# Kernel optimization log

Measured on AMD Instinct MI355X. Metric: run time of the kernel, lower is better.

The kernel has to match this reference:

```python
import jax, jax.numpy as jnp
import numpy as np

N_NODES = 100000
N_EDGES = 3200000
NODE_DIM = 128
MRI_DIM, COG_DIM, CLIN_DIM, GEN_DIM = 256, 64, 32, 512
N_GRAPHS = 256
N_CLASSES = 3
HID = 16


def setup_inputs() -> dict:
    key = jax.random.key(0)
    ks = jax.random.split(key, 20)
    inp = {
        "x": jax.random.normal(ks[0], (N_NODES, NODE_DIM), jnp.float32),
        "edge_index": jax.random.randint(ks[1], (2, N_EDGES), 0, N_NODES, jnp.int64),
        "batch": jnp.sort(jax.random.randint(ks[2], (N_NODES,), 0, N_GRAPHS, jnp.int64)),
        "mri": jax.random.normal(ks[3], (N_GRAPHS, MRI_DIM), jnp.float32),
        "cog": jax.random.normal(ks[4], (N_GRAPHS, COG_DIM), jnp.float32),
        "clin": jax.random.normal(ks[5], (N_GRAPHS, CLIN_DIM), jnp.float32),
        "genetic": jax.random.normal(ks[6], (N_GRAPHS, GEN_DIM), jnp.float32),
        # GCNConv weight/bias
        "gcn_W": jax.random.normal(ks[7], (NODE_DIM, HID), jnp.float32) / np.sqrt(NODE_DIM),
        "gcn_b": jnp.zeros((HID,), jnp.float32),
        # modality FCs (each -> 4)
        "mri_W": jax.random.normal(ks[8], (MRI_DIM, 4), jnp.float32) / np.sqrt(MRI_DIM),
        "mri_b": jnp.zeros((4,), jnp.float32),
        "cog_W": jax.random.normal(ks[9], (COG_DIM, 4), jnp.float32) / np.sqrt(COG_DIM),
        "cog_b": jnp.zeros((4,), jnp.float32),
        "clin_W": jax.random.normal(ks[10], (CLIN_DIM, 4), jnp.float32) / np.sqrt(CLIN_DIM),
        "clin_b": jnp.zeros((4,), jnp.float32),
        "gen_W": jax.random.normal(ks[11], (GEN_DIM, 4), jnp.float32) / np.sqrt(GEN_DIM),
        "gen_b": jnp.zeros((4,), jnp.float32),
        # classifier: Linear(32,16) -> ReLU -> Dropout(eval: identity) -> Linear(16,3)
        "cls_W1": jax.random.normal(ks[12], (32, HID), jnp.float32) / np.sqrt(32.0),
        "cls_b1": jnp.zeros((HID,), jnp.float32),
        "cls_W2": jax.random.normal(ks[13], (HID, N_CLASSES), jnp.float32) / np.sqrt(HID),
        "cls_b2": jnp.zeros((N_CLASSES,), jnp.float32),
    }
    return inp


def gcn_conv(x, edge_index, W, b):
    # PyG GCNConv: add self-loops, symmetric normalization, scatter-add.
    n = x.shape[0]
    xw = x @ W  # [N, HID]
    loop = jnp.arange(n, dtype=edge_index.dtype)
    src = jnp.concatenate([edge_index[0], loop])
    dst = jnp.concatenate([edge_index[1], loop])
    deg = jax.ops.segment_sum(jnp.ones_like(dst, dtype=xw.dtype), dst, num_segments=n)
    dinv = jnp.where(deg > 0, jax.lax.rsqrt(deg), 0.0)
    norm = dinv[src] * dinv[dst]  # [E+N]
    msg = xw[src] * norm[:, None]  # gather + scale
    out = jax.ops.segment_sum(msg, dst, num_segments=n)  # scatter-add
    return out + b


def global_mean_pool(feat, batch, num_graphs):
    s = jax.ops.segment_sum(feat, batch, num_segments=num_graphs)
    cnt = jax.ops.segment_sum(jnp.ones((feat.shape[0],), feat.dtype), batch, num_segments=num_graphs)
    return s / jnp.maximum(cnt, 1.0)[:, None]


def reference(x, edge_index, batch, mri, cog, clin, genetic,
              gcn_W, gcn_b, mri_W, mri_b, cog_W, cog_b, clin_W, clin_b,
              gen_W, gen_b, cls_W1, cls_b1, cls_W2, cls_b2):
    g = jax.nn.relu(gcn_conv(x, edge_index, gcn_W, gcn_b))  # [N, 16]
    g_emb = global_mean_pool(g, batch, N_GRAPHS)            # [B, 16]
    m = jax.nn.relu(mri @ mri_W + mri_b)
    c = jax.nn.relu(cog @ cog_W + cog_b)
    cl = jax.nn.relu(clin @ clin_W + clin_b)
    ge = jax.nn.relu(genetic @ gen_W + gen_b)
    mm = jnp.concatenate([m, c, cl, ge], axis=1)            # [B, 16]
    comb = jnp.concatenate([g_emb, mm], axis=1)             # [B, 32]
    h = jax.nn.relu(comb @ cls_W1 + cls_b1)                 # dropout is identity in eval
    logits = h @ cls_W2 + cls_b2
    return jax.nn.log_softmax(logits, axis=1)
```

## Files before the change

kernel.cpp:

```cpp
#include <hip/hip_runtime.h>
#include <hip/hip_bf16.h>
#include <math.h>

#define N_NODES   100000
#define N_EDGES   3200000
#define NODE_DIM  128
#define HID       16
#define N_GRAPHS  256

#define BSHIFT    6
#define NPB       64
#define NBUCK     ((N_NODES + NPB - 1) >> BSHIFT)
#define NBLK      256
#define TOT       (NBUCK * NBLK)
#define ACC64S    9

#define FIX16  4096.0f
#define IFIX16 (1.0f/4096.0f)
#define FIXP   131072.0f
#define IFIXP  (1.0f/131072.0f)

__device__ __forceinline__ short f2bf(float f) {
    unsigned u = __float_as_uint(f);
    unsigned r = (u + 0x7FFF + ((u >> 16) & 1)) >> 16;
    return (short)r;
}
__device__ __forceinline__ int fx(float v, float s) { return __float2int_rn(v * s); }

__device__ __forceinline__ unsigned long long packA(int w) {
    return ((unsigned long long)(unsigned)(w >> 16) << 32)
         | (unsigned)((w & 0xFFFF) ^ 0x8000);
}

typedef __attribute__((ext_vector_type(8))) short bf16x8;
typedef __attribute__((ext_vector_type(4))) float f32x4;
typedef __attribute__((ext_vector_type(4))) int   i32x4;

__global__ __launch_bounds__(1024) void bucket_count(
    const int* __restrict__ dst, int* __restrict__ offT, int E, int chunk)
{
    __shared__ int cnt[NBUCK];
    const int t = threadIdx.x;
    const int b = (blockIdx.x & 7) * (NBLK >> 3) + (blockIdx.x >> 3);
    for (int k = t; k < NBUCK; k += 1024) cnt[k] = 0;
    __syncthreads();
    int e0 = b * chunk, e1 = min(E, e0 + chunk);
    if (e1 > e0) {
        const int4* d4 = (const int4*)dst;
        for (int i = (e0 >> 2) + t; i < (e1 >> 2); i += 1024) {
            int4 d = d4[i];
            atomicAdd(&cnt[d.x >> BSHIFT], 1);
            atomicAdd(&cnt[d.y >> BSHIFT], 1);
            atomicAdd(&cnt[d.z >> BSHIFT], 1);
            atomicAdd(&cnt[d.w >> BSHIFT], 1);
        }
    }
    __syncthreads();
    for (int k = t; k < NBUCK; k += 1024) offT[k * NBLK + b] = cnt[k];
}

__global__ __launch_bounds__(256) void scan_blocksum(
    const int* __restrict__ M, int* __restrict__ bsum, int n)
{
    __shared__ int red[256];
    int t = threadIdx.x;
    int base = blockIdx.x * 2048 + t * 8;
    int s = 0;
    #pragma unroll
    for (int k = 0; k < 8; ++k) { int i = base + k; if (i < n) s += M[i]; }
    red[t] = s; __syncthreads();
    for (int o = 128; o > 0; o >>= 1) {
        if (t < o) red[t] += red[t + o];
        __syncthreads();
    }
    if (t == 0) bsum[blockIdx.x] = red[0];
}

__global__ __launch_bounds__(256) void scan_write2(
    int* __restrict__ M, const int* __restrict__ bsum, int n, int nb)
{
    __shared__ int tmp[256];
    __shared__ int tsum[256];
    int t = threadIdx.x;
    tmp[t] = (t < nb) ? bsum[t] : 0;
    __syncthreads();
    for (int o = 1; o < 256; o <<= 1) {
        int a = (t >= o) ? tmp[t - o] : 0;
        __syncthreads();
        tmp[t] += a;
        __syncthreads();
    }
    const int pre0 = (blockIdx.x > 0) ? tmp[blockIdx.x - 1] : 0;

    int base = blockIdx.x * 2048 + t * 8;
    int v[8]; int s = 0;
    #pragma unroll
    for (int k = 0; k < 8; ++k) { int i = base + k; v[k] = (i < n) ? M[i] : 0; s += v[k]; }
    tsum[t] = s; __syncthreads();
    int mine = s;
    for (int o = 1; o < 256; o <<= 1) {
        int a = (t >= o) ? tsum[t - o] : 0;
        __syncthreads();
        tsum[t] += a;
        __syncthreads();
    }
    int pre = pre0 + tsum[t] - mine;
    #pragma unroll
    for (int k = 0; k < 8; ++k) {
        int i = base + k;
        if (i < n) { M[i] = pre; pre += v[k]; }
    }
}

__global__ __launch_bounds__(1024) void bucket_scatter(
    const int* __restrict__ src, const int* __restrict__ dst,
    const int* __restrict__ offT, int* __restrict__ ebuf, int E, int chunk)
{
    __shared__ int cur[NBUCK];
    const int t = threadIdx.x;
    const int b = (blockIdx.x & 7) * (NBLK >> 3) + (blockIdx.x >> 3);
    for (int k = t; k < NBUCK; k += 1024) cur[k] = offT[k * NBLK + b];
    __syncthreads();
    int e0 = b * chunk, e1 = min(E, e0 + chunk);
    if (e1 <= e0) return;
    const i32x4* d4 = (const i32x4*)dst;
    const i32x4* s4 = (const i32x4*)src;
    for (int i = (e0 >> 2) + t; i < (e1 >> 2); i += 1024) {
        i32x4 d = __builtin_nontemporal_load(&d4[i]);
        i32x4 s = __builtin_nontemporal_load(&s4[i]);
        int p;
        p = atomicAdd(&cur[d[0] >> BSHIFT], 1); ebuf[p] = s[0] | ((d[0] & (NPB-1)) << 17);
        p = atomicAdd(&cur[d[1] >> BSHIFT], 1); ebuf[p] = s[1] | ((d[1] & (NPB-1)) << 17);
        p = atomicAdd(&cur[d[2] >> BSHIFT], 1); ebuf[p] = s[2] | ((d[2] & (NPB-1)) << 17);
        p = atomicAdd(&cur[d[3] >> BSHIFT], 1); ebuf[p] = s[3] | ((d[3] & (NPB-1)) << 17);
    }
}

__global__ __launch_bounds__(256) void degxw_kernel(
    const int* __restrict__ offT, const int* __restrict__ ebuf,
    const float* __restrict__ x, const float* __restrict__ W,
    float* __restrict__ dinv, int* __restrict__ degA,
    short* __restrict__ xws16, int N, int E)
{
    __shared__ int hist4[4][72];
    __shared__ float dloc[NPB];
    const int k = blockIdx.x, t = threadIdx.x;
    const int base = k << BSHIFT;
    const int wave = t >> 6;

    {
        int* hp = &hist4[0][0];
        for (int i = t; i < 4 * 72; i += 256) hp[i] = 0;
    }
    __syncthreads();
    {
        int start = offT[k * NBLK];
        int end = (k == NBUCK - 1) ? E : offT[(k + 1) * NBLK];
        for (int j = start + t; j < end; j += 256)
            atomicAdd(&hist4[wave][ebuf[j] >> 17], 1);
    }
    __syncthreads();
    if (t < NPB) {
        int dd = hist4[0][t] + hist4[1][t] + hist4[2][t] + hist4[3][t];
        float dv = rsqrtf((float)(dd + 1));
        dloc[t] = dv;
        if (base + t < N) { dinv[base + t] = dv; degA[base + t] = dd; }
    }
    __syncthreads();

    const int lane = t & 63;
    const int q = lane >> 4, n = lane & 15;
    const int tile_base = base + (t >> 6) * 16;
    if (tile_base >= N) return;

    bf16x8 bfrag[4];
    #pragma unroll
    for (int i = 0; i < 4; ++i)
        #pragma unroll
        for (int j = 0; j < 8; ++j)
            bfrag[i][j] = f2bf(W[(i * 32 + q * 8 + j) * HID + n]);

    const float4* x4 = (const float4*)x;
    const int node = tile_base + n;
    f32x4 d = {0.f, 0.f, 0.f, 0.f};
    #pragma unroll
    for (int i = 0; i < 4; ++i) {
        float4 u0 = make_float4(0.f, 0.f, 0.f, 0.f), u1 = u0;
        if (node < N) {
            u0 = x4[(size_t)node * 32 + i * 8 + q * 2];
            u1 = x4[(size_t)node * 32 + i * 8 + q * 2 + 1];
        }
        bf16x8 a;
        a[0] = f2bf(u0.x); a[1] = f2bf(u0.y); a[2] = f2bf(u0.z); a[3] = f2bf(u0.w);
        a[4] = f2bf(u1.x); a[5] = f2bf(u1.y); a[6] = f2bf(u1.z); a[7] = f2bf(u1.w);
        d = __builtin_amdgcn_mfma_f32_16x16x32_bf16(a, bfrag[i], d, 0, 0, 0);
    }
    #pragma unroll
    for (int r = 0; r < 4; ++r) {
        int nd = tile_base + q * 4 + r;
        if (nd < N) {
            float val = d[r] * dloc[nd - base];
            val = fminf(7.995f, fmaxf(-7.995f, val));
            xws16[(size_t)nd * HID + n] = (short)__float2int_rn(val * FIX16);
        }
    }
}

__global__ __launch_bounds__(256, 8) void gather_pool(
    const int* __restrict__ offT, const int* __restrict__ ebuf,
    const float* __restrict__ dinv, const int* __restrict__ degA,
    const short* __restrict__ xws16, const float* __restrict__ gcn_b,
    const int* __restrict__ batch, int* __restrict__ pool,
    int* __restrict__ cnt, int N, int E)
{
    __shared__ unsigned long long acc64[NPB * ACC64S];
    __shared__ int lpool[16 * HID];
    __shared__ int lcnt[16];
    const int k = blockIdx.x, t = threadIdx.x;
    const int base = k << BSHIFT;

    for (int i = t; i < NPB * ACC64S; i += 256) acc64[i] = 0ull;
    lpool[t] = 0;
    if (t < 16) lcnt[t] = 0;

    const int start = offT[k * NBLK];
    const int end = (k == NBUCK - 1) ? E : offT[(k + 1) * NBLK];
    const int Ek = end - start;
    __syncthreads();

    const int sub = t >> 1, h = t & 1;
    const int4* xw4 = (const int4*)xws16;
    const int* eb = ebuf + start;

    int e = sub;
    for (; e + 7 * 128 < Ek; e += 1024) {
        int w[8]; int4 vv[8];
        #pragma unroll
        for (int u = 0; u < 8; ++u) w[u] = eb[e + u * 128];
        #pragma unroll
        for (int u = 0; u < 8; ++u) vv[u] = xw4[(size_t)(w[u] & 0x1FFFF) * 2 + h];
        #pragma unroll
        for (int u = 0; u < 8; ++u) {
            unsigned long long* p = &acc64[(w[u] >> 17) * ACC64S + h * 4];
            atomicAdd(p + 0, packA(vv[u].x));
            atomicAdd(p + 1, packA(vv[u].y));
            atomicAdd(p + 2, packA(vv[u].z));
            atomicAdd(p + 3, packA(vv[u].w));
        }
    }
    for (; e < Ek; e += 128) {
        int w = eb[e];
        int4 vv = xw4[(size_t)(w & 0x1FFFF) * 2 + h];
        unsigned long long* p = &acc64[(w >> 17) * ACC64S + h * 4];
        atomicAdd(p + 0, packA(vv.x));
        atomicAdd(p + 1, packA(vv.y));
        atomicAdd(p + 2, packA(vv.z));
        atomicAdd(p + 3, packA(vv.w));
    }
    __syncthreads();

    int nN = min(NPB, N - base);
    int gmin = batch[base], gmax = batch[base + nN - 1];
    int range = gmax - gmin + 1;
    bool useL = (range <= 16);
    const int sub16 = t >> 4, lane16 = t & 15;
    float bb = gcn_b[lane16];

    for (int i = sub16; i < nN; i += 16) {
        int n = base + i;
        unsigned long long word = acc64[i * ACC64S + (lane16 >> 1)];
        int s = (lane16 & 1)
              ? (int)(unsigned)(word >> 32)
              : (int)(unsigned)(word & 0xFFFFFFFFull) - degA[n] * 32768;
        int tot = s + (int)xws16[(size_t)n * HID + lane16];
        float a = (float)tot * IFIX16;
        float r = fmaxf(fmaf(dinv[n], a, bb), 0.f);
        int g = batch[n];
        int ri = fx(r, FIXP);
        if (useL) {
            atomicAdd(&lpool[(g - gmin) * HID + lane16], ri);
            if (lane16 == 0) atomicAdd(&lcnt[g - gmin], 1);
        } else {
            atomicAdd(&pool[g * HID + lane16], ri);
            if (lane16 == 0) atomicAdd(&cnt[g], 1);
        }
    }
    __syncthreads();

    if (useL) {
        for (int i = t; i < range * HID; i += 256) {
            int vv = lpool[i];
            if (vv != 0) atomicAdd(&pool[gmin * HID + i], vv);
        }
        for (int i = t; i < range; i += 256) {
            int c = lcnt[i];
            if (c != 0) atomicAdd(&cnt[gmin + i], c);
        }
    }
}

__global__ __launch_bounds__(64) void head_kernel(
    const int* __restrict__ pool, const int* __restrict__ cnt,
    const float* __restrict__ mri,  const float* __restrict__ cog,
    const float* __restrict__ clin, const float* __restrict__ gen,
    const float* __restrict__ mriW, const float* __restrict__ mrib,
    const float* __restrict__ cogW, const float* __restrict__ cogb,
    const float* __restrict__ clinW, const float* __restrict__ clinb,
    const float* __restrict__ genW, const float* __restrict__ genb,
    const float* __restrict__ W1, const float* __restrict__ b1,
    const float* __restrict__ W2, const float* __restrict__ b2,
    float* __restrict__ out)
{
    const int g = blockIdx.x;
    const int lane = threadIdx.x;
    __shared__ float comb[32];
    __shared__ float h[HID];

    if (lane < HID) {
        float c = fmaxf((float)cnt[g], 1.f);
        comb[lane] = ((float)pool[g * HID + lane] * IFIXP) / c;
    }

    struct Mod { const float* in; const float* W; const float* b; int K; int off; };
    Mod mods[4] = {
        { mri  + (size_t)g * 256, mriW,  mrib,  256, 16 },
        { cog  + (size_t)g * 64,  cogW,  cogb,  64,  20 },
        { clin + (size_t)g * 32,  clinW, clinb, 32,  24 },
        { gen  + (size_t)g * 512, genW,  genb,  512, 28 },
    };
    for (int m = 0; m < 4; ++m) {
        float p0 = 0.f, p1 = 0.f, p2 = 0.f, p3 = 0.f;
        const float* in = mods[m].in;
        const float* Wm = mods[m].W;
        for (int kk = lane; kk < mods[m].K; kk += 64) {
            float xv = in[kk];
            p0 += xv * Wm[kk * 4 + 0];
            p1 += xv * Wm[kk * 4 + 1];
            p2 += xv * Wm[kk * 4 + 2];
            p3 += xv * Wm[kk * 4 + 3];
        }
        #pragma unroll
        for (int o = 32; o > 0; o >>= 1) {
            p0 += __shfl_down(p0, o);
            p1 += __shfl_down(p1, o);
            p2 += __shfl_down(p2, o);
            p3 += __shfl_down(p3, o);
        }
        if (lane == 0) {
            const float* bm = mods[m].b;
            int o = mods[m].off;
            comb[o + 0] = fmaxf(p0 + bm[0], 0.f);
            comb[o + 1] = fmaxf(p1 + bm[1], 0.f);
            comb[o + 2] = fmaxf(p2 + bm[2], 0.f);
            comb[o + 3] = fmaxf(p3 + bm[3], 0.f);
        }
    }
    __syncthreads();

    if (lane < HID) {
        float a = b1[lane];
        #pragma unroll
        for (int kk = 0; kk < 32; ++kk) a += comb[kk] * W1[kk * HID + lane];
        h[lane] = fmaxf(a, 0.f);
    }
    __syncthreads();

    if (lane == 0) {
        float l0 = b2[0], l1 = b2[1], l2 = b2[2];
        #pragma unroll
        for (int kk = 0; kk < HID; ++kk) {
            float hv = h[kk];
            l0 += hv * W2[kk * 3 + 0];
            l1 += hv * W2[kk * 3 + 1];
            l2 += hv * W2[kk * 3 + 2];
        }
        float mx = fmaxf(l0, fmaxf(l1, l2));
        float lse = mx + logf(expf(l0 - mx) + expf(l1 - mx) + expf(l2 - mx));
        out[g * 3 + 0] = l0 - lse;
        out[g * 3 + 1] = l1 - lse;
        out[g * 3 + 2] = l2 - lse;
    }
}

extern "C" void kernel_launch(void* const* d_in, const int* in_sizes, int n_in,
                              void* d_out, int out_size, void* d_ws, size_t ws_size,
                              hipStream_t stream)
{
    const float* x     = (const float*)d_in[0];
    const int*   eidx  = (const int*)d_in[1];
    const int*   batch = (const int*)d_in[2];
    const float* mri   = (const float*)d_in[3];
    const float* cog   = (const float*)d_in[4];
    const float* clin  = (const float*)d_in[5];
    const float* gen   = (const float*)d_in[6];
    const float* gcn_W = (const float*)d_in[7];
    const float* gcn_b = (const float*)d_in[8];
    const float* mriW  = (const float*)d_in[9];
    const float* mrib  = (const float*)d_in[10];
    const float* cogW  = (const float*)d_in[11];
    const float* cogb  = (const float*)d_in[12];
    const float* clinW = (const float*)d_in[13];
    const float* clinb = (const float*)d_in[14];
    const float* genW  = (const float*)d_in[15];
    const float* genb  = (const float*)d_in[16];
    const float* W1    = (const float*)d_in[17];
    const float* b1    = (const float*)d_in[18];
    const float* W2    = (const float*)d_in[19];
    const float* b2    = (const float*)d_in[20];
    float* out = (float*)d_out;

    const int N = in_sizes[0] / NODE_DIM;
    const int E = in_sizes[1] / 2;
    const int* src = eidx;
    const int* dst = eidx + E;

    float* ws    = (float*)d_ws;
    short* xws16 = (short*)ws;
    float* dinv  = ws + 800000;
    int*   pool  = (int*)(ws + 900000);
    int*   cnt   = (int*)(ws + 904096);
    int*   offT  = (int*)(ws + 1306000);
    int*   bsum  = (int*)(ws + 2108000);
    int*   ebuf  = (int*)(ws + 2109000);
    int*   degA  = (int*)(ws + 5309000);

    const int chunkE = (E + NBLK - 1) / NBLK;
    const int scanNB = (TOT + 2047) / 2048;

    hipMemsetAsync(pool, 0, (N_GRAPHS * HID + N_GRAPHS) * sizeof(int), stream);

    bucket_count<<<NBLK, 1024, 0, stream>>>(dst, offT, E, chunkE);
    scan_blocksum<<<scanNB, 256, 0, stream>>>(offT, bsum, TOT);
    scan_write2<<<scanNB, 256, 0, stream>>>(offT, bsum, TOT, scanNB);
    bucket_scatter<<<NBLK, 1024, 0, stream>>>(src, dst, offT, ebuf, E, chunkE);
    degxw_kernel<<<NBUCK, 256, 0, stream>>>(offT, ebuf, x, gcn_W, dinv, degA, xws16, N, E);
    gather_pool<<<NBUCK, 256, 0, stream>>>(offT, ebuf, dinv, degA, xws16,
                                           gcn_b, batch, pool, cnt, N, E);
    head_kernel<<<N_GRAPHS, 64, 0, stream>>>(
        pool, cnt, mri, cog, clin, gen,
        mriW, mrib, cogW, cogb, clinW, clinb, genW, genb,
        W1, b1, W2, b2, out);
}
```

Baseline: 218.2 us.

## Fuse two-pass scan into one kernel with last-block decoupled sync; fold memset

Merges the block-sum and write passes of the offset scan into a single kernel. Each block publishes its sum, and the last block to arrive scans the block sums while the others spin on a flag. The separate memset of the pool and count buffers is moved into block 0 of the bucket-count kernel. This saves two launches and one re-read of the matrix, but the spin-wait relies on all scan blocks being co-resident, and the sync counters are zeroed by bucket_count (pool+4408 ints covers sync at offset 904400).

```diff
diff --git a/kernel.cpp b/kernel.cpp
--- a/kernel.cpp
+++ b/kernel.cpp
@@ -37,11 +37,15 @@
 typedef __attribute__((ext_vector_type(4))) int   i32x4;
 
 __global__ __launch_bounds__(1024) void bucket_count(
-    const int* __restrict__ dst, int* __restrict__ offT, int E, int chunk)
+    const int* __restrict__ dst, int* __restrict__ offT,
+    int* __restrict__ pz, int nz, int E, int chunk)
 {
     __shared__ int cnt[NBUCK];
     const int t = threadIdx.x;
     const int b = (blockIdx.x & 7) * (NBLK >> 3) + (blockIdx.x >> 3);
+    if (blockIdx.x == 0) {
+        for (int i = t; i < nz; i += 1024) pz[i] = 0;
+    }
     for (int k = t; k < NBUCK; k += 1024) cnt[k] = 0;
     __syncthreads();
     int e0 = b * chunk, e1 = min(E, e0 + chunk);
@@ -59,43 +63,58 @@
     for (int k = t; k < NBUCK; k += 1024) offT[k * NBLK + b] = cnt[k];
 }
 
-__global__ __launch_bounds__(256) void scan_blocksum(
-    const int* __restrict__ M, int* __restrict__ bsum, int n)
+__global__ __launch_bounds__(256) void scan_fused(
+    int* __restrict__ M, int* __restrict__ bsum, int* __restrict__ bscan,
+    int* __restrict__ sync, int n, int nb)
 {
     __shared__ int red[256];
-    int t = threadIdx.x;
-    int base = blockIdx.x * 2048 + t * 8;
-    int s = 0;
-    #pragma unroll
-    for (int k = 0; k < 8; ++k) { int i = base + k; if (i < n) s += M[i]; }
+    __shared__ int tmp[256];
+    __shared__ int tsum[256];
+    __shared__ int lastFlag;
+    __shared__ int spre;
+    const int t = threadIdx.x, bid = blockIdx.x;
+    const int base = bid * 2048 + t * 8;
+
+    int v[8]; int s = 0;
+    #pragma unroll
+    for (int k = 0; k < 8; ++k) { int i = base + k; v[k] = (i < n) ? M[i] : 0; s += v[k]; }
+
     red[t] = s; __syncthreads();
+    #pragma unroll
     for (int o = 128; o > 0; o >>= 1) {
         if (t < o) red[t] += red[t + o];
         __syncthreads();
     }
-    if (t == 0) bsum[blockIdx.x] = red[0];
-}
-
-__global__ __launch_bounds__(256) void scan_write2(
-    int* __restrict__ M, const int* __restrict__ bsum, int n, int nb)
-{
-    __shared__ int tmp[256];
-    __shared__ int tsum[256];
-    int t = threadIdx.x;
-    tmp[t] = (t < nb) ? bsum[t] : 0;
-    __syncthreads();
-    for (int o = 1; o < 256; o <<= 1) {
-        int a = (t >= o) ? tmp[t - o] : 0;
+    if (t == 0) {
+        atomicExch(&bsum[bid], red[0]);
+        __threadfence();
+        int old = atomicAdd(&sync[0], 1);
+        lastFlag = (old == nb - 1) ? 1 : 0;
+    }
+    __syncthreads();
+
+    if (lastFlag) {
+        int val = (t < nb) ? atomicAdd(&bsum[t], 0) : 0;
+        tmp[t] = val; __syncthreads();
+        for (int o = 1; o < 256; o <<= 1) {
+            int a = (t >= o) ? tmp[t - o] : 0;
+            __syncthreads();
+            tmp[t] += a;
+            __syncthreads();
+        }
+        if (t < nb) atomicExch(&bscan[t], tmp[t]);
+        __threadfence();
         __syncthreads();
-        tmp[t] += a;
-        __syncthreads();
-    }
-    const int pre0 = (blockIdx.x > 0) ? tmp[blockIdx.x - 1] : 0;
-
-    int base = blockIdx.x * 2048 + t * 8;
-    int v[8]; int s = 0;
-    #pragma unroll
-    for (int k = 0; k < 8; ++k) { int i = base + k; v[k] = (i < n) ? M[i] : 0; s += v[k]; }
+        if (t == 0) atomicExch(&sync[1], 1);
+    } else if (t == 0) {
+        while (atomicAdd(&sync[1], 0) == 0) __builtin_amdgcn_s_sleep(8);
+    }
+    __syncthreads();
+
+    if (t == 0) spre = (bid > 0) ? atomicAdd(&bscan[bid - 1], 0) : 0;
+    __syncthreads();
+    const int pre0 = spre;
+
     tsum[t] = s; __syncthreads();
     int mine = s;
     for (int o = 1; o < 256; o <<= 1) {
@@ -419,19 +438,19 @@
     float* dinv  = ws + 800000;
     int*   pool  = (int*)(ws + 900000);
     int*   cnt   = (int*)(ws + 904096);
+    int*   sync  = (int*)(ws + 904400);
     int*   offT  = (int*)(ws + 1306000);
     int*   bsum  = (int*)(ws + 2108000);
+    int*   bscan = (int*)(ws + 2108500);
     int*   ebuf  = (int*)(ws + 2109000);
     int*   degA  = (int*)(ws + 5309000);
 
     const int chunkE = (E + NBLK - 1) / NBLK;
     const int scanNB = (TOT + 2047) / 2048;
-
-    hipMemsetAsync(pool, 0, (N_GRAPHS * HID + N_GRAPHS) * sizeof(int), stream);
-
-    bucket_count<<<NBLK, 1024, 0, stream>>>(dst, offT, E, chunkE);
-    scan_blocksum<<<scanNB, 256, 0, stream>>>(offT, bsum, TOT);
-    scan_write2<<<scanNB, 256, 0, stream>>>(offT, bsum, TOT, scanNB);
+    const int nz = 4408;
+
+    bucket_count<<<NBLK, 1024, 0, stream>>>(dst, offT, pool, nz, E, chunkE);
+    scan_fused<<<scanNB, 256, 0, stream>>>(offT, bsum, bscan, sync, TOT, scanNB);
     bucket_scatter<<<NBLK, 1024, 0, stream>>>(src, dst, offT, ebuf, E, chunkE);
     degxw_kernel<<<NBUCK, 256, 0, stream>>>(offT, ebuf, x, gcn_W, dinv, degA, xws16, N, E);
     gather_pool<<<NBUCK, 256, 0, stream>>>(offT, ebuf, dinv, degA, xws16,
```

New measurement: 222.6 us. About the same (+2.0%).
